# Kernel tuning notes

Measured on AMD Instinct MI355X. Metric: run time of the kernel, lower is better.

The kernel has to match this reference:

```python
import jax, jax.numpy as jnp
import numpy as np

# Model dims (match init_kwargs)
X = 256   # input_size
H = 512   # num_units
R = 128   # r_size
M = 128   # mem_cap
TAU = 1.0
F_BIAS = 1.0
T = 256   # timesteps
B = 256   # batch


def setup_inputs() -> dict:
    key = jax.random.key(0)
    ks = jax.random.split(key, 10)
    return {
        "x": jax.random.normal(ks[0], (T, B, X), jnp.float32),
        "noise": jax.random.uniform(ks[1], (T, B, M), jnp.float32),
        "W_full": jax.random.normal(ks[2], (X + R + H, R + 4 * H), jnp.float32) * 0.05,
        "bias": jnp.zeros((R + 4 * H,), jnp.float32),
        "W_full1": jax.random.normal(ks[3], (X + R + H, R + H), jnp.float32) * 0.05,
        "bias1": jnp.zeros((R + H,), jnp.float32),
        "fc_w": jax.random.normal(ks[4], (M, X + H), jnp.float32) * 0.05,
        "fc_b": jnp.zeros((M,), jnp.float32),
        "trans_w": jax.random.normal(ks[5], (R, H), jnp.float32) * 0.05,
        "trans_b": jnp.zeros((R,), jnp.float32),
        "c_bias": jax.random.normal(ks[6], (1, H), jnp.float32),
        "hmem_bias": jnp.zeros((1, M, R), jnp.float32),
    }


def _armin_scan(x, noise, W_full, bias, W_full1, bias1, fc_w, fc_b,
                trans_w, trans_b, c_bias, hmem_bias):
    c0 = jnp.tanh(jnp.broadcast_to(c_bias, (B, H)))
    hmem0 = jnp.broadcast_to(hmem_bias, (B, M, R)) + jnp.zeros((B, M, R), x.dtype)

    def step(carry, inp):
        c, hmem = carry
        x_t, g_t, t = inp
        # read head: fc([x, c]) -> [B, M]
        head = jnp.concatenate([x_t, c], axis=1) @ fc_w.T + fc_b
        # gumbel-softmax with straight-through hard one-hot
        gumbel = -jnp.log(1e-20 - jnp.log(1e-20 + g_t))
        y = jax.nn.softmax((head + gumbel) * TAU, axis=1)
        hard = jax.nn.one_hot(jnp.argmax(y, axis=1), M, dtype=y.dtype)
        h_index = jax.lax.stop_gradient(hard - y) + y          # [B, M]
        h_entry = jnp.einsum('bm,bmr->br', h_index, hmem)      # memory read [B, R]
        # gated cell
        concat = jnp.concatenate([x_t, c, h_entry], axis=1)    # [B, X+H+R]
        gates1 = jax.nn.sigmoid(concat @ W_full1 + bias1)      # [B, R+H]
        concat = concat * jnp.concatenate([jnp.ones_like(x_t), gates1], axis=1)
        pre = concat @ W_full + bias                           # [B, R+4H]
        i, j, f, o = pre[:, :H], pre[:, H:2*H], pre[:, 2*H:3*H], pre[:, 3*H:4*H]
        om = pre[:, 4*H:]                                      # [B, R] (remainder chunk)
        new_c = jnp.tanh(c * jax.nn.sigmoid(f + F_BIAS)
                         + jax.nn.sigmoid(i) * jnp.tanh(j))
        new_h = new_c * jax.nn.sigmoid(o)
        r = h_entry * jax.nn.sigmoid(om)
        # write: sequential fill while memcnt < mem_cap, else last read slot
        fill = jax.nn.one_hot(t, M, dtype=y.dtype)[None, :]
        w_idx = jnp.where(t < M, fill, jax.lax.stop_gradient(h_index))[..., None]
        wv = new_c @ trans_w.T + trans_b                       # [B, R]
        hmem = wv[:, None, :] * w_idx + hmem * (1.0 - w_idx)
        return (new_c, hmem), jnp.concatenate([new_h, r], axis=1)

    (_, _), outs = jax.lax.scan(step, (c0, hmem0), (x, noise, jnp.arange(T)))
    return outs  # [T, B, H+R]


def reference(x, noise, W_full, bias, W_full1, bias1, fc_w, fc_b,
              trans_w, trans_b, c_bias, hmem_bias):
    return _armin_scan(x, noise, W_full, bias, W_full1, bias1, fc_w, fc_b,
                       trans_w, trans_b, c_bias, hmem_bias)
```

## Files before the change

### kernel.cpp

```cpp
#include <hip/hip_runtime.h>
#include <cmath>


#define TT 256
#define BB 256
#define XD 256
#define HD 512
#define RD 128
#define MD 128
#define N1 640
#define NP 2176

#define OFF_C     0u
#define OFF_HMEM  131072u
#define OFF_HENT  4325376u
#define OFF_SEL   4358144u
#define OFF_FXT   4358400u
#define OFF_TWT   4391168u
#define OFF_FWT   4456704u
#define OFF_HEAD0 4522240u
#define OFF_G1P   4522496u
#define OFF_PREP  4850176u

#define NBLK 136

__device__ unsigned int g_flag[NBLK];
__device__ unsigned int g_rel;
__device__ unsigned int g_abrt;

__device__ __forceinline__ float sigm(float z){ return 1.0f/(1.0f + expf(-z)); }
__device__ __forceinline__ float4 ld4(const float* p){ return *(const float4*)p; }

__global__ __launch_bounds__(256)
void k_pre(const float* __restrict__ fc_w, const float* __restrict__ trans_w,
           const float* __restrict__ c_bias, const float* __restrict__ hmem_bias,
           float* __restrict__ ws)
{
  float*  cbuf   = ws + OFF_C;
  float*  hmem   = ws + OFF_HMEM;
  float*  fcxT   = ws + OFF_FXT;
  float*  transT = ws + OFF_TWT;
  float*  fcwcT  = ws + OFF_FWT;
  double* head0d = (double*)(ws + OFF_HEAD0);

  const int gt = blockIdx.x*256 + threadIdx.x, GT = gridDim.x*256;
  if (blockIdx.x == 0 && threadIdx.x < NBLK) g_flag[threadIdx.x] = 0u;
  if (gt == 0) { g_rel = 0u; g_abrt = 0u; }
  for (int i = gt; i < BB*HD;    i += GT) cbuf[i] = (float)tanh((double)c_bias[i & 511]);
  for (int i = gt; i < BB*MD*RD; i += GT) hmem[i] = hmem_bias[i & (MD*RD - 1)];
  for (int i = gt; i < XD*128;   i += GT) { int k=i>>7, m=i&127; fcxT[i]  = fc_w[(size_t)m*768 + k]; }
  for (int i = gt; i < HD*128;   i += GT) { int k=i>>7, o=i&127; transT[i] = trans_w[(size_t)o*512 + k];
                                            fcwcT[i]  = fc_w[(size_t)o*768 + 256 + k]; }
  if (blockIdx.x == 0 && threadIdx.x < 128) {
    double a = 0.0;
    for (int k = 0; k < 512; ++k)
      a += tanh((double)c_bias[k]) * (double)fc_w[(size_t)threadIdx.x*768 + 256 + k];
    head0d[threadIdx.x] = a;
  }
}

__global__ __launch_bounds__(256)
void k_score(const float* __restrict__ x, const float* __restrict__ noise,
             const float* __restrict__ fc_b, const float* __restrict__ ws_fcxT,
             float* __restrict__ out)
{
  __shared__ float xs[16*256];
  const int tid = threadIdx.x;
  const int rbase = blockIdx.x * 16;
  for (int i = tid; i < 16*64; i += 256) {
    int row = i >> 6, kq = (i & 63) << 2;
    *(float4*)&xs[row*256 + kq] = ld4(x + (size_t)(rbase + row)*XD + kq);
  }
  __syncthreads();
  const int m = tid & 127, r0 = (tid >> 7) * 8;
  double acc[8] = {};
  for (int k = 0; k < 256; ++k) {
    double wk = (double)ws_fcxT[k*128 + m];
    #pragma unroll
    for (int r = 0; r < 8; ++r) acc[r] += wk * (double)xs[(r0+r)*256 + k];
  }
  #pragma unroll
  for (int r = 0; r < 8; ++r) {
    size_t grow = (size_t)rbase + r0 + r;
    double g   = (double)noise[grow*MD + m];
    double gum = -log(1e-20 - log(1e-20 + g));
    out[grow*640 + 512 + m] = (float)(acc[r] + (double)fc_b[m] + gum);
  }
}

__global__ __launch_bounds__(256)
void k_scan(const float* __restrict__ x, const float* __restrict__ W_full,
            const float* __restrict__ W_full1, const float* __restrict__ bias,
            const float* __restrict__ bias1, const float* __restrict__ trans_b,
            float* __restrict__ out, float* __restrict__ ws)
{
  __shared__ float As[16][68];
  __shared__ float Bs[16][128];
  __shared__ int   sel[64];
  __shared__ float smc[4*512];
  __shared__ float smwv[4*128];
  __shared__ int   s_bad;

  const int tid = threadIdx.x, bid = blockIdx.x;
  unsigned int bars = 0;

  auto gbar = [&]() -> bool {
    ++bars;
    if (tid == 0) s_bad = 0;
    __syncthreads();
    if (tid == 0)
      __hip_atomic_store(&g_flag[bid], bars, __ATOMIC_RELEASE, __HIP_MEMORY_SCOPE_AGENT);
    if (bid == 0) {
      if (tid < NBLK) {
        long long t0 = __builtin_amdgcn_s_memrealtime();
        while (__hip_atomic_load(&g_flag[tid], __ATOMIC_RELAXED, __HIP_MEMORY_SCOPE_AGENT) < bars) {
          __builtin_amdgcn_s_sleep(1);
          if (__hip_atomic_load(&g_abrt, __ATOMIC_RELAXED, __HIP_MEMORY_SCOPE_AGENT) != 0u ||
              __builtin_amdgcn_s_memrealtime() - t0 > 20000000LL) {
            __hip_atomic_store(&g_abrt, 1u, __ATOMIC_RELAXED, __HIP_MEMORY_SCOPE_AGENT);
            s_bad = 1; break;
          }
        }
      }
      __syncthreads();
      if (tid == 0) {
        if (s_bad == 0)
          __hip_atomic_store(&g_rel, bars, __ATOMIC_RELEASE, __HIP_MEMORY_SCOPE_AGENT);
        __threadfence();
      }
      __syncthreads();
      return s_bad == 0;
    } else {
      if (tid == 0) {
        long long t0 = __builtin_amdgcn_s_memrealtime();
        while (__hip_atomic_load(&g_rel, __ATOMIC_RELAXED, __HIP_MEMORY_SCOPE_AGENT) < bars) {
          __builtin_amdgcn_s_sleep(1);
          if (__hip_atomic_load(&g_abrt, __ATOMIC_RELAXED, __HIP_MEMORY_SCOPE_AGENT) != 0u ||
              __builtin_amdgcn_s_memrealtime() - t0 > 25000000LL) {
            __hip_atomic_store(&g_abrt, 1u, __ATOMIC_RELAXED, __HIP_MEMORY_SCOPE_AGENT);
            s_bad = 1; break;
          }
        }
        __threadfence();
      }
      __syncthreads();
      return s_bad == 0;
    }
  };

  for (int t = 0; t < TT; ++t) {
    if (bid < 80) {
      const int rt = bid & 3, ct = (bid >> 2) % 10, kc = bid / 40;
      const int r0 = rt*64, n0 = ct*64, kbeg = kc*448;
      const float* cbuf = ws + OFF_C;
      const float* hmem = ws + OFF_HMEM;
      float*  hent  = ws + OFF_HENT;
      int*    selb  = (int*)(ws + OFF_SEL);
      double* head0d= (double*)(ws + OFF_HEAD0);
      float*  g1p   = ws + OFF_G1P + (size_t)kc*BB*N1;

      if (kc == 1) {
        if (tid < 64) {
          const float* sc = out + ((size_t)t*BB + r0 + tid)*640 + 512;
          int bi = 0;
          if (t == 0) { double best = -1e300;
            for (int m = 0; m < 128; ++m) { double v = (double)sc[m] + head0d[m]; if (v > best) { best = v; bi = m; } } }
          else { float best = -3.4e38f;
            for (int m = 0; m < 128; ++m) { float v = sc[m]; if (v > best) { best = v; bi = m; } } }
          sel[tid] = bi;
        }
        __syncthreads();
        if (ct == 0) {
          if (tid < 64) selb[r0 + tid] = sel[tid];
          for (int idx = tid; idx < 64*128; idx += 256) {
            int row = idx >> 7, rr = idx & 127;
            hent[(size_t)(r0+row)*RD + rr] = hmem[((size_t)(r0+row)*MD + sel[row])*RD + rr];
          }
        }
      }

      float  acc[4][4] = {};
      double accd[4][4] = {};
      const int tx = tid & 15, ty = tid >> 4;
      const int arow = tid >> 2, akq = (tid & 3) << 2;
      const int bkk = tid >> 4, bnq = (tid & 15) << 2;

      for (int k0 = kbeg; k0 < kbeg + 448; k0 += 16) {
        __syncthreads();
        {
          int b = r0 + arow, k = k0 + akq;
          float4 v;
          if (k < XD)           v = ld4(x + ((size_t)t*BB + b)*XD + k);
          else if (k < XD + HD) v = ld4(cbuf + (size_t)b*HD + (k - XD));
          else                  v = ld4(hmem + ((size_t)b*MD + sel[arow])*RD + (k - (XD+HD)));
          As[akq+0][arow] = v.x; As[akq+1][arow] = v.y;
          As[akq+2][arow] = v.z; As[akq+3][arow] = v.w;
        }
        *(float4*)&Bs[bkk][bnq] = ld4(W_full1 + (size_t)(k0 + bkk)*N1 + n0 + bnq);
        __syncthreads();
        #pragma unroll
        for (int kk = 0; kk < 16; ++kk) {
          float a[4], b[4];
          *(float4*)a = ld4(&As[kk][ty*4]);
          *(float4*)b = ld4(&Bs[kk][tx*4]);
          #pragma unroll
          for (int i = 0; i < 4; ++i)
            #pragma unroll
            for (int j = 0; j < 4; ++j)
              acc[i][j] = fmaf(a[i], b[j], acc[i][j]);
          if ((kk & 7) == 7) {
            #pragma unroll
            for (int i = 0; i < 4; ++i)
              #pragma unroll
              for (int j = 0; j < 4; ++j) { accd[i][j] += (double)acc[i][j]; acc[i][j] = 0.f; }
          }
        }
      }
      #pragma unroll
      for (int i = 0; i < 4; ++i)
        #pragma unroll
        for (int j = 0; j < 4; ++j)
          g1p[(size_t)(r0 + ty*4 + i)*N1 + n0 + tx*4 + j] = (float)accd[i][j];
    }
    if (!gbar()) return;

    {
      const int rt = bid & 3, ct = (bid >> 2) % 17, kc = bid / 68;
      const int r0 = rt*64, n0 = ct*128, kbeg = kc*448;
      const float* cbuf = ws + OFF_C;
      const float* hent = ws + OFF_HENT;
      const float* g1p0 = ws + OFF_G1P;
      const float* g1p1 = g1p0 + (size_t)BB*N1;
      float* prep = ws + OFF_PREP + (size_t)kc*BB*NP;

      float  acc[4][8] = {};
      double accd[4][8] = {};
      const int tx = tid & 15, ty = tid >> 4;
      const int arow = tid >> 2, akq = (tid & 3) << 2;

      for (int k0 = kbeg; k0 < kbeg + 448; k0 += 16) {
        __syncthreads();
        {
          int b = r0 + arow, k = k0 + akq;
          float4 v;
          if (k < XD) v = ld4(x + ((size_t)t*BB + b)*XD + k);
          else if (k < XD + HD) {
            int j = k - XD;
            v = ld4(cbuf + (size_t)b*HD + j);
            float4 p0 = ld4(g1p0 + (size_t)b*N1 + j);
            float4 p1 = ld4(g1p1 + (size_t)b*N1 + j);
            float4 bb = ld4(bias1 + j);
            v.x *= sigm(p0.x + p1.x + bb.x);
            v.y *= sigm(p0.y + p1.y + bb.y);
            v.z *= sigm(p0.z + p1.z + bb.z);
            v.w *= sigm(p0.w + p1.w + bb.w);
          } else {
            int j = k - (XD + HD);
            v = ld4(hent + (size_t)b*RD + j);
            float4 p0 = ld4(g1p0 + (size_t)b*N1 + 512 + j);
            float4 p1 = ld4(g1p1 + (size_t)b*N1 + 512 + j);
            float4 bb = ld4(bias1 + 512 + j);
            v.x *= sigm(p0.x + p1.x + bb.x);
            v.y *= sigm(p0.y + p1.y + bb.y);
            v.z *= sigm(p0.z + p1.z + bb.z);
            v.w *= sigm(p0.w + p1.w + bb.w);
          }
          As[akq+0][arow] = v.x; As[akq+1][arow] = v.y;
          As[akq+2][arow] = v.z; As[akq+3][arow] = v.w;
        }
        #pragma unroll
        for (int rep = 0; rep < 2; ++rep) {
          int idx = tid + rep*256, kk = idx >> 5, nq = (idx & 31) << 2;
          *(float4*)&Bs[kk][nq] = ld4(W_full + (size_t)(k0 + kk)*NP + n0 + nq);
        }
        __syncthreads();
        #pragma unroll
        for (int kk = 0; kk < 16; ++kk) {
          float a[4], b[8];
          *(float4*)a = ld4(&As[kk][ty*4]);
          *(float4*)&b[0] = ld4(&Bs[kk][tx*8]);
          *(float4*)&b[4] = ld4(&Bs[kk][tx*8 + 4]);
          #pragma unroll
          for (int i = 0; i < 4; ++i)
            #pragma unroll
            for (int j = 0; j < 8; ++j)
              acc[i][j] = fmaf(a[i], b[j], acc[i][j]);
          if ((kk & 7) == 7) {
            #pragma unroll
            for (int i = 0; i < 4; ++i)
              #pragma unroll
              for (int j = 0; j < 8; ++j) { accd[i][j] += (double)acc[i][j]; acc[i][j] = 0.f; }
          }
        }
      }
      #pragma unroll
      for (int i = 0; i < 4; ++i)
        #pragma unroll
        for (int j = 0; j < 8; ++j)
          prep[(size_t)(r0 + ty*4 + i)*NP + n0 + tx*8 + j] = (float)accd[i][j];
    }
    if (!gbar()) return;

    if (bid < 64) {
      const int b0 = bid*4;
      float*  cbuf   = ws + OFF_C;
      float*  hmem   = ws + OFF_HMEM;
      float*  hent   = ws + OFF_HENT;
      int*    selb   = (int*)(ws + OFF_SEL);
      float*  transT = ws + OFF_TWT;
      float*  fcwcT  = ws + OFF_FWT;
      const float* prep0 = ws + OFF_PREP;
      const float* prep1 = prep0 + (size_t)BB*NP;

      for (int idx = tid; idx < 4*512; idx += 256) {
        int br = idx >> 9, hh = idx & 511, b = b0 + br;
        const float* p0 = prep0 + (size_t)b*NP;
        const float* p1 = prep1 + (size_t)b*NP;
        float iv = p0[hh]        + p1[hh]        + bias[hh];
        float jv = p0[512 + hh]  + p1[512 + hh]  + bias[512 + hh];
        float fv = p0[1024 + hh] + p1[1024 + hh] + bias[1024 + hh];
        float ov = p0[1536 + hh] + p1[1536 + hh] + bias[1536 + hh];
        float cold = cbuf[(size_t)b*HD + hh];
        float nc = tanhf(cold*sigm(fv + 1.0f) + sigm(iv)*tanhf(jv));
        cbuf[(size_t)b*HD + hh] = nc;
        smc[br*512 + hh] = nc;
        out[((size_t)t*BB + b)*640 + hh] = nc * sigm(ov);
      }
      for (int idx = tid; idx < 4*128; idx += 256) {
        int br = idx >> 7, rr = idx & 127, b = b0 + br;
        float om = prep0[(size_t)b*NP + 2048 + rr] + prep1[(size_t)b*NP + 2048 + rr] + bias[2048 + rr];
        out[((size_t)t*BB + b)*640 + 512 + rr] = hent[(size_t)b*RD + rr] * sigm(om);
      }
      __syncthreads();
      if (t < TT-1) {
        int o = tid & 127, mat = tid >> 7;
        const float* WT = mat ? fcwcT : transT;
        double a0=0., a1=0., a2=0., a3=0.;
        for (int k = 0; k < 512; k += 4) {
          float w0 = WT[(k+0)*128 + o], w1 = WT[(k+1)*128 + o];
          float w2 = WT[(k+2)*128 + o], w3 = WT[(k+3)*128 + o];
          float4 c0v = ld4(&smc[0*512 + k]);
          float4 c1v = ld4(&smc[1*512 + k]);
          float4 c2v = ld4(&smc[2*512 + k]);
          float4 c3v = ld4(&smc[3*512 + k]);
          a0 += (double)w0*c0v.x + (double)w1*c0v.y + (double)w2*c0v.z + (double)w3*c0v.w;
          a1 += (double)w0*c1v.x + (double)w1*c1v.y + (double)w2*c1v.z + (double)w3*c1v.w;
          a2 += (double)w0*c2v.x + (double)w1*c2v.y + (double)w2*c2v.z + (double)w3*c2v.w;
          a3 += (double)w0*c3v.x + (double)w1*c3v.y + (double)w2*c3v.z + (double)w3*c3v.w;
        }
        if (mat == 0) {
          smwv[0*128+o] = (float)(a0 + (double)trans_b[o]);
          smwv[1*128+o] = (float)(a1 + (double)trans_b[o]);
          smwv[2*128+o] = (float)(a2 + (double)trans_b[o]);
          smwv[3*128+o] = (float)(a3 + (double)trans_b[o]);
        } else {
          float* sx = out + ((size_t)(t+1)*BB)*640;
          sx[(size_t)(b0+0)*640 + 512 + o] = (float)((double)sx[(size_t)(b0+0)*640 + 512 + o] + a0);
          sx[(size_t)(b0+1)*640 + 512 + o] = (float)((double)sx[(size_t)(b0+1)*640 + 512 + o] + a1);
          sx[(size_t)(b0+2)*640 + 512 + o] = (float)((double)sx[(size_t)(b0+2)*640 + 512 + o] + a2);
          sx[(size_t)(b0+3)*640 + 512 + o] = (float)((double)sx[(size_t)(b0+3)*640 + 512 + o] + a3);
        }
        __syncthreads();
        for (int idx = tid; idx < 4*128; idx += 256) {
          int br = idx >> 7, rr = idx & 127, b = b0 + br;
          int slot = (t < MD) ? t : selb[b];
          hmem[((size_t)b*MD + slot)*RD + rr] = smwv[br*128 + rr];
        }
      }
    }
    if (!gbar()) return;
  }
}

extern "C" void kernel_launch(void* const* d_in, const int* in_sizes, int n_in,
                              void* d_out, int out_size, void* d_ws, size_t ws_size,
                              hipStream_t stream) {
  const float* x         = (const float*)d_in[0];
  const float* noise     = (const float*)d_in[1];
  const float* W_full    = (const float*)d_in[2];
  const float* bias      = (const float*)d_in[3];
  const float* W_full1   = (const float*)d_in[4];
  const float* bias1     = (const float*)d_in[5];
  const float* fc_w      = (const float*)d_in[6];
  const float* fc_b      = (const float*)d_in[7];
  const float* trans_w   = (const float*)d_in[8];
  const float* trans_b   = (const float*)d_in[9];
  const float* c_bias    = (const float*)d_in[10];
  const float* hmem_bias = (const float*)d_in[11];
  float* out = (float*)d_out;
  float* ws  = (float*)d_ws;

  k_pre  <<<dim3(256),  dim3(256), 0, stream>>>(fc_w, trans_w, c_bias, hmem_bias, ws);
  k_score<<<dim3(4096), dim3(256), 0, stream>>>(x, noise, fc_b, ws + OFF_FXT, out);
  k_scan <<<dim3(NBLK), dim3(256), 0, stream>>>(x, W_full, W_full1, bias, bias1,
                                                trans_b, out, ws);
}
```

Measured before the change: 43.86 ms.

## Spread persistent scan across more blocks with smaller tiles and double-buffered loads

Grows the persistent scan grid from 136 to 320 blocks and halves the row tile from 64 to 32 in both GEMM phases, so more CUs share each timestep's work. Adds register-prefetch double buffering of the shared-memory tiles and pads the barrier flags to one per cache line. The cell-update phase now covers 2 rows per block across 128 blocks. The cost is a grid barrier over more participants and smaller per-block tiles with less reuse, and the launch config must match the new block count.

```diff
diff --git a/kernel.cpp b/kernel.cpp
--- a/kernel.cpp
+++ b/kernel.cpp
@@ -22,9 +22,9 @@
 #define OFF_G1P   4522496u
 #define OFF_PREP  4850176u
 
-#define NBLK 136
-
-__device__ unsigned int g_flag[NBLK];
+#define NBLK 320
+
+__device__ unsigned int g_flag[NBLK * 16];
 __device__ unsigned int g_rel;
 __device__ unsigned int g_abrt;
 
@@ -44,7 +44,7 @@
   double* head0d = (double*)(ws + OFF_HEAD0);
 
   const int gt = blockIdx.x*256 + threadIdx.x, GT = gridDim.x*256;
-  if (blockIdx.x == 0 && threadIdx.x < NBLK) g_flag[threadIdx.x] = 0u;
+  for (int i = gt; i < NBLK*16; i += GT) g_flag[i] = 0u;
   if (gt == 0) { g_rel = 0u; g_abrt = 0u; }
   for (int i = gt; i < BB*HD;    i += GT) cbuf[i] = (float)tanh((double)c_bias[i & 511]);
   for (int i = gt; i < BB*MD*RD; i += GT) hmem[i] = hmem_bias[i & (MD*RD - 1)];
@@ -88,20 +88,21 @@
   }
 }
 
-__global__ __launch_bounds__(256)
+__global__ __launch_bounds__(256, 2)
 void k_scan(const float* __restrict__ x, const float* __restrict__ W_full,
             const float* __restrict__ W_full1, const float* __restrict__ bias,
             const float* __restrict__ bias1, const float* __restrict__ trans_b,
             float* __restrict__ out, float* __restrict__ ws)
 {
-  __shared__ float As[16][68];
-  __shared__ float Bs[16][128];
-  __shared__ int   sel[64];
-  __shared__ float smc[4*512];
-  __shared__ float smwv[4*128];
+  __shared__ float As[2][16][36];
+  __shared__ float Bs[2][16][128];
+  __shared__ int   sel[32];
+  __shared__ float smc[2*512];
+  __shared__ float smwv[2*128];
   __shared__ int   s_bad;
 
   const int tid = threadIdx.x, bid = blockIdx.x;
+  const int x8 = bid & 7, s8 = bid >> 3;
   unsigned int bars = 0;
 
   auto gbar = [&]() -> bool {
@@ -109,11 +110,11 @@
     if (tid == 0) s_bad = 0;
     __syncthreads();
     if (tid == 0)
-      __hip_atomic_store(&g_flag[bid], bars, __ATOMIC_RELEASE, __HIP_MEMORY_SCOPE_AGENT);
+      __hip_atomic_store(&g_flag[bid*16], bars, __ATOMIC_RELEASE, __HIP_MEMORY_SCOPE_AGENT);
     if (bid == 0) {
-      if (tid < NBLK) {
+      for (int f = tid; f < NBLK; f += 256) {
         long long t0 = __builtin_amdgcn_s_memrealtime();
-        while (__hip_atomic_load(&g_flag[tid], __ATOMIC_RELAXED, __HIP_MEMORY_SCOPE_AGENT) < bars) {
+        while (__hip_atomic_load(&g_flag[f*16], __ATOMIC_RELAXED, __HIP_MEMORY_SCOPE_AGENT) < bars) {
           __builtin_amdgcn_s_sleep(1);
           if (__hip_atomic_load(&g_abrt, __ATOMIC_RELAXED, __HIP_MEMORY_SCOPE_AGENT) != 0u ||
               __builtin_amdgcn_s_memrealtime() - t0 > 20000000LL) {
@@ -121,6 +122,7 @@
             s_bad = 1; break;
           }
         }
+        if (s_bad) break;
       }
       __syncthreads();
       if (tid == 0) {
@@ -148,19 +150,28 @@
     }
   };
 
+  const int m8 = s8 >> 3;
+  const int rt = s8 & 7;
+  const int c1 = x8 + (m8 << 3);
+  const bool p1_act = (s8 < 24) && (c1 < 20);
+  const int ct1 = c1 % 10, kc1 = c1 / 10;
+  const int c2 = x8 + (m8 << 3);
+  const bool p2_act = (c2 < 34);
+  const int ct2 = c2 % 17, kc2 = c2 / 17;
+
+  float* cbuf = ws + OFF_C;
+  float* hmem = ws + OFF_HMEM;
+  float* hent = ws + OFF_HENT;
+  int*   selb = (int*)(ws + OFF_SEL);
+  double* head0d = (double*)(ws + OFF_HEAD0);
+
   for (int t = 0; t < TT; ++t) {
-    if (bid < 80) {
-      const int rt = bid & 3, ct = (bid >> 2) % 10, kc = bid / 40;
-      const int r0 = rt*64, n0 = ct*64, kbeg = kc*448;
-      const float* cbuf = ws + OFF_C;
-      const float* hmem = ws + OFF_HMEM;
-      float*  hent  = ws + OFF_HENT;
-      int*    selb  = (int*)(ws + OFF_SEL);
-      double* head0d= (double*)(ws + OFF_HEAD0);
-      float*  g1p   = ws + OFF_G1P + (size_t)kc*BB*N1;
-
-      if (kc == 1) {
-        if (tid < 64) {
+    if (p1_act) {
+      const int r0 = rt*32, n0 = ct1*64, kbeg = kc1*448;
+      float* g1p = ws + OFF_G1P + (size_t)kc1*BB*N1;
+
+      if (kc1 == 1) {
+        if (tid < 32) {
           const float* sc = out + ((size_t)t*BB + r0 + tid)*640 + 512;
           int bi = 0;
           if (t == 0) { double best = -1e300;
@@ -170,149 +181,168 @@
           sel[tid] = bi;
         }
         __syncthreads();
-        if (ct == 0) {
-          if (tid < 64) selb[r0 + tid] = sel[tid];
-          for (int idx = tid; idx < 64*128; idx += 256) {
+        if (ct1 == 0) {
+          if (tid < 32) selb[r0 + tid] = sel[tid];
+          for (int idx = tid; idx < 32*128; idx += 256) {
             int row = idx >> 7, rr = idx & 127;
             hent[(size_t)(r0+row)*RD + rr] = hmem[((size_t)(r0+row)*MD + sel[row])*RD + rr];
           }
         }
       }
 
-      float  acc[4][4] = {};
-      double accd[4][4] = {};
       const int tx = tid & 15, ty = tid >> 4;
-      const int arow = tid >> 2, akq = (tid & 3) << 2;
+      const int ar = tid >> 2, aq = (tid & 3) << 2;
       const int bkk = tid >> 4, bnq = (tid & 15) << 2;
 
-      for (int k0 = kbeg; k0 < kbeg + 448; k0 += 16) {
-        __syncthreads();
-        {
-          int b = r0 + arow, k = k0 + akq;
-          float4 v;
-          if (k < XD)           v = ld4(x + ((size_t)t*BB + b)*XD + k);
-          else if (k < XD + HD) v = ld4(cbuf + (size_t)b*HD + (k - XD));
-          else                  v = ld4(hmem + ((size_t)b*MD + sel[arow])*RD + (k - (XD+HD)));
-          As[akq+0][arow] = v.x; As[akq+1][arow] = v.y;
-          As[akq+2][arow] = v.z; As[akq+3][arow] = v.w;
-        }
-        *(float4*)&Bs[bkk][bnq] = ld4(W_full1 + (size_t)(k0 + bkk)*N1 + n0 + bnq);
-        __syncthreads();
+      float4 va, vb;
+      auto issue1 = [&](int k0) {
+        if (tid < 128) {
+          int b = r0 + ar, k = k0 + aq;
+          if (k < XD)           va = ld4(x + ((size_t)t*BB + b)*XD + k);
+          else if (k < XD + HD) va = ld4(cbuf + (size_t)b*HD + (k - XD));
+          else                  va = ld4(hmem + ((size_t)b*MD + sel[ar])*RD + (k - (XD+HD)));
+        }
+        vb = ld4(W_full1 + (size_t)(k0 + bkk)*N1 + n0 + bnq);
+      };
+      auto write1 = [&](int buf) {
+        if (tid < 128) {
+          As[buf][aq+0][ar] = va.x; As[buf][aq+1][ar] = va.y;
+          As[buf][aq+2][ar] = va.z; As[buf][aq+3][ar] = va.w;
+        }
+        *(float4*)&Bs[buf][bkk][bnq] = vb;
+      };
+
+      float  acc[2][4] = {};
+      double accd[2][4] = {};
+      int cur = 0;
+      issue1(kbeg); write1(0);
+      __syncthreads();
+      for (int it = 0; it < 28; ++it) {
+        const bool pf = (it + 1 < 28);
+        if (pf) issue1(kbeg + (it+1)*16);
         #pragma unroll
         for (int kk = 0; kk < 16; ++kk) {
-          float a[4], b[4];
-          *(float4*)a = ld4(&As[kk][ty*4]);
-          *(float4*)b = ld4(&Bs[kk][tx*4]);
+          float a[2], b[4];
+          *(float2*)a = *(const float2*)&As[cur][kk][ty*2];
+          *(float4*)b = ld4(&Bs[cur][kk][tx*4]);
           #pragma unroll
-          for (int i = 0; i < 4; ++i)
+          for (int i = 0; i < 2; ++i)
             #pragma unroll
             for (int j = 0; j < 4; ++j)
               acc[i][j] = fmaf(a[i], b[j], acc[i][j]);
           if ((kk & 7) == 7) {
             #pragma unroll
-            for (int i = 0; i < 4; ++i)
+            for (int i = 0; i < 2; ++i)
               #pragma unroll
               for (int j = 0; j < 4; ++j) { accd[i][j] += (double)acc[i][j]; acc[i][j] = 0.f; }
           }
         }
+        if (pf) write1(cur ^ 1);
+        __syncthreads();
+        cur ^= 1;
       }
       #pragma unroll
-      for (int i = 0; i < 4; ++i)
+      for (int i = 0; i < 2; ++i)
         #pragma unroll
         for (int j = 0; j < 4; ++j)
-          g1p[(size_t)(r0 + ty*4 + i)*N1 + n0 + tx*4 + j] = (float)accd[i][j];
+          g1p[(size_t)(r0 + ty*2 + i)*N1 + n0 + tx*4 + j] = (float)accd[i][j];
     }
     if (!gbar()) return;
 
-    {
-      const int rt = bid & 3, ct = (bid >> 2) % 17, kc = bid / 68;
-      const int r0 = rt*64, n0 = ct*128, kbeg = kc*448;
-      const float* cbuf = ws + OFF_C;
-      const float* hent = ws + OFF_HENT;
+    if (p2_act) {
+      const int r0 = rt*32, n0 = ct2*128, kbeg = kc2*448;
       const float* g1p0 = ws + OFF_G1P;
       const float* g1p1 = g1p0 + (size_t)BB*N1;
-      float* prep = ws + OFF_PREP + (size_t)kc*BB*NP;
-
-      float  acc[4][8] = {};
-      double accd[4][8] = {};
+      float* prep = ws + OFF_PREP + (size_t)kc2*BB*NP;
+
       const int tx = tid & 15, ty = tid >> 4;
-      const int arow = tid >> 2, akq = (tid & 3) << 2;
-
-      for (int k0 = kbeg; k0 < kbeg + 448; k0 += 16) {
-        __syncthreads();
-        {
-          int b = r0 + arow, k = k0 + akq;
-          float4 v;
-          if (k < XD) v = ld4(x + ((size_t)t*BB + b)*XD + k);
+      const int ar = tid >> 2, aq = (tid & 3) << 2;
+
+      float4 va, p0v, p1v, bbv, vb0, vb1;
+      int areg = 0;
+      auto issue2 = [&](int k0) {
+        if (tid < 128) {
+          int b = r0 + ar, k = k0 + aq;
+          if (k < XD) { areg = 0; va = ld4(x + ((size_t)t*BB + b)*XD + k); }
           else if (k < XD + HD) {
-            int j = k - XD;
-            v = ld4(cbuf + (size_t)b*HD + j);
-            float4 p0 = ld4(g1p0 + (size_t)b*N1 + j);
-            float4 p1 = ld4(g1p1 + (size_t)b*N1 + j);
-            float4 bb = ld4(bias1 + j);
-            v.x *= sigm(p0.x + p1.x + bb.x);
-            v.y *= sigm(p0.y + p1.y + bb.y);
-            v.z *= sigm(p0.z + p1.z + bb.z);
-            v.w *= sigm(p0.w + p1.w + bb.w);
+            int j = k - XD; areg = 1;
+            va  = ld4(cbuf + (size_t)b*HD + j);
+            p0v = ld4(g1p0 + (size_t)b*N1 + j);
+            p1v = ld4(g1p1 + (size_t)b*N1 + j);
+            bbv = ld4(bias1 + j);
           } else {
-            int j = k - (XD + HD);
-            v = ld4(hent + (size_t)b*RD + j);
-            float4 p0 = ld4(g1p0 + (size_t)b*N1 + 512 + j);
-            float4 p1 = ld4(g1p1 + (size_t)b*N1 + 512 + j);
-            float4 bb = ld4(bias1 + 512 + j);
-            v.x *= sigm(p0.x + p1.x + bb.x);
-            v.y *= sigm(p0.y + p1.y + bb.y);
-            v.z *= sigm(p0.z + p1.z + bb.z);
-            v.w *= sigm(p0.w + p1.w + bb.w);
-          }
-          As[akq+0][arow] = v.x; As[akq+1][arow] = v.y;
-          As[akq+2][arow] = v.z; As[akq+3][arow] = v.w;
-        }
-        #pragma unroll
-        for (int rep = 0; rep < 2; ++rep) {
-          int idx = tid + rep*256, kk = idx >> 5, nq = (idx & 31) << 2;
-          *(float4*)&Bs[kk][nq] = ld4(W_full + (size_t)(k0 + kk)*NP + n0 + nq);
-        }
-        __syncthreads();
+            int j = k - (XD + HD); areg = 1;
+            va  = ld4(hent + (size_t)b*RD + j);
+            p0v = ld4(g1p0 + (size_t)b*N1 + 512 + j);
+            p1v = ld4(g1p1 + (size_t)b*N1 + 512 + j);
+            bbv = ld4(bias1 + 512 + j);
+          }
+        }
+        vb0 = ld4(W_full + (size_t)(k0 + (tid>>5))*NP + n0 + ((tid&31)<<2));
+        vb1 = ld4(W_full + (size_t)(k0 + (tid>>5) + 8)*NP + n0 + ((tid&31)<<2));
+      };
+      auto write2 = [&](int buf) {
+        if (tid < 128) {
+          float4 v = va;
+          if (areg) {
+            v.x *= sigm(p0v.x + p1v.x + bbv.x);
+            v.y *= sigm(p0v.y + p1v.y + bbv.y);
+            v.z *= sigm(p0v.z + p1v.z + bbv.z);
+            v.w *= sigm(p0v.w + p1v.w + bbv.w);
+          }
+          As[buf][aq+0][ar] = v.x; As[buf][aq+1][ar] = v.y;
+          As[buf][aq+2][ar] = v.z; As[buf][aq+3][ar] = v.w;
+        }
+        *(float4*)&Bs[buf][tid>>5][(tid&31)<<2] = vb0;
+        *(float4*)&Bs[buf][(tid>>5) + 8][(tid&31)<<2] = vb1;
+      };
+
+      float  acc[2][8] = {};
+      double accd[2][8] = {};
+      int cur = 0;
+      issue2(kbeg); write2(0);
+      __syncthreads();
+      for (int it = 0; it < 28; ++it) {
+        const bool pf = (it + 1 < 28);
+        if (pf) issue2(kbeg + (it+1)*16);
         #pragma unroll
         for (int kk = 0; kk < 16; ++kk) {
-          float a[4], b[8];
-          *(float4*)a = ld4(&As[kk][ty*4]);
-          *(float4*)&b[0] = ld4(&Bs[kk][tx*8]);
-          *(float4*)&b[4] = ld4(&Bs[kk][tx*8 + 4]);
+          float a[2], b[8];
+          *(float2*)a = *(const float2*)&As[cur][kk][ty*2];
+          *(float4*)&b[0] = ld4(&Bs[cur][kk][tx*8]);
+          *(float4*)&b[4] = ld4(&Bs[cur][kk][tx*8 + 4]);
           #pragma unroll
-          for (int i = 0; i < 4; ++i)
+          for (int i = 0; i < 2; ++i)
             #pragma unroll
             for (int j = 0; j < 8; ++j)
               acc[i][j] = fmaf(a[i], b[j], acc[i][j]);
           if ((kk & 7) == 7) {
             #pragma unroll
-            for (int i = 0; i < 4; ++i)
+            for (int i = 0; i < 2; ++i)
               #pragma unroll
               for (int j = 0; j < 8; ++j) { accd[i][j] += (double)acc[i][j]; acc[i][j] = 0.f; }
           }
         }
+        if (pf) write2(cur ^ 1);
+        __syncthreads();
+        cur ^= 1;
       }
       #pragma unroll
-      for (int i = 0; i < 4; ++i)
+      for (int i = 0; i < 2; ++i)
         #pragma unroll
         for (int j = 0; j < 8; ++j)
-          prep[(size_t)(r0 + ty*4 + i)*NP + n0 + tx*8 + j] = (float)accd[i][j];
+          prep[(size_t)(r0 + ty*2 + i)*NP + n0 + tx*8 + j] = (float)accd[i][j];
     }
     if (!gbar()) return;
 
-    if (bid < 64) {
-      const int b0 = bid*4;
-      float*  cbuf   = ws + OFF_C;
-      float*  hmem   = ws + OFF_HMEM;
-      float*  hent   = ws + OFF_HENT;
-      int*    selb   = (int*)(ws + OFF_SEL);
+    if (bid < 128) {
+      const int b0 = bid*2;
       float*  transT = ws + OFF_TWT;
       float*  fcwcT  = ws + OFF_FWT;
       const float* prep0 = ws + OFF_PREP;
       const float* prep1 = prep0 + (size_t)BB*NP;
 
-      for (int idx = tid; idx < 4*512; idx += 256) {
+      for (int idx = tid; idx < 2*512; idx += 256) {
         int br = idx >> 9, hh = idx & 511, b = b0 + br;
         const float* p0 = prep0 + (size_t)b*NP;
         const float* p1 = prep1 + (size_t)b*NP;
@@ -326,7 +356,7 @@
         smc[br*512 + hh] = nc;
         out[((size_t)t*BB + b)*640 + hh] = nc * sigm(ov);
       }
-      for (int idx = tid; idx < 4*128; idx += 256) {
+      for (int idx = tid; idx < 2*128; idx += 256) {
         int br = idx >> 7, rr = idx & 127, b = b0 + br;
         float om = prep0[(size_t)b*NP + 2048 + rr] + prep1[(size_t)b*NP + 2048 + rr] + bias[2048 + rr];
         out[((size_t)t*BB + b)*640 + 512 + rr] = hent[(size_t)b*RD + rr] * sigm(om);
@@ -335,33 +365,25 @@
       if (t < TT-1) {
         int o = tid & 127, mat = tid >> 7;
         const float* WT = mat ? fcwcT : transT;
-        double a0=0., a1=0., a2=0., a3=0.;
+        double a0=0., a1=0.;
         for (int k = 0; k < 512; k += 4) {
           float w0 = WT[(k+0)*128 + o], w1 = WT[(k+1)*128 + o];
           float w2 = WT[(k+2)*128 + o], w3 = WT[(k+3)*128 + o];
           float4 c0v = ld4(&smc[0*512 + k]);
           float4 c1v = ld4(&smc[1*512 + k]);
-          float4 c2v = ld4(&smc[2*512 + k]);
-          float4 c3v = ld4(&smc[3*512 + k]);
           a0 += (double)w0*c0v.x + (double)w1*c0v.y + (double)w2*c0v.z + (double)w3*c0v.w;
           a1 += (double)w0*c1v.x + (double)w1*c1v.y + (double)w2*c1v.z + (double)w3*c1v.w;
-          a2 += (double)w0*c2v.x + (double)w1*c2v.y + (double)w2*c2v.z + (double)w3*c2v.w;
-          a3 += (double)w0*c3v.x + (double)w1*c3v.y + (double)w2*c3v.z + (double)w3*c3v.w;
         }
         if (mat == 0) {
           smwv[0*128+o] = (float)(a0 + (double)trans_b[o]);
           smwv[1*128+o] = (float)(a1 + (double)trans_b[o]);
-          smwv[2*128+o] = (float)(a2 + (double)trans_b[o]);
-          smwv[3*128+o] = (float)(a3 + (double)trans_b[o]);
         } else {
           float* sx = out + ((size_t)(t+1)*BB)*640;
           sx[(size_t)(b0+0)*640 + 512 + o] = (float)((double)sx[(size_t)(b0+0)*640 + 512 + o] + a0);
           sx[(size_t)(b0+1)*640 + 512 + o] = (float)((double)sx[(size_t)(b0+1)*640 + 512 + o] + a1);
-          sx[(size_t)(b0+2)*640 + 512 + o] = (float)((double)sx[(size_t)(b0+2)*640 + 512 + o] + a2);
-          sx[(size_t)(b0+3)*640 + 512 + o] = (float)((double)sx[(size_t)(b0+3)*640 + 512 + o] + a3);
         }
         __syncthreads();
-        for (int idx = tid; idx < 4*128; idx += 256) {
+        for (int idx = tid; idx < 2*128; idx += 256) {
           int br = idx >> 7, rr = idx & 127, b = b0 + br;
           int slot = (t < MD) ? t : selb[b];
           hmem[((size_t)b*MD + slot)*RD + rr] = smwv[br*128 + rr];
```

After: 40.92 ms. 1.07x faster.
